# Kernel optimization log

Hardware: AMD Instinct MI355X
Metric: run time of the kernel (lower is better)

## Reference

```python
import jax, jax.numpy as jnp
import numpy as np

NUM_HEADS = 32
NUM_KV_HEADS = 8
HEAD_DIM = 128
ROPE_BASE = 10000.0


def rotate_half(x):
    half = x.shape[-1] // 2
    x1, x2 = x[..., :half], x[..., half:]
    return jnp.concatenate((-x2, x1), axis=-1)


def rope_cos_sin(position_ids, head_dim, dtype):
    # inv_freq: [head_dim/2]
    inv_freq = 1.0 / (ROPE_BASE ** (jnp.arange(0, head_dim, 2, dtype=jnp.float32) / head_dim))
    freqs = position_ids.astype(jnp.float32)[..., None] * inv_freq  # [B, S, hd/2]
    emb = jnp.concatenate((freqs, freqs), axis=-1)                  # [B, S, hd]
    # add head axis -> [B, 1, S, hd]
    return jnp.cos(emb)[:, None].astype(dtype), jnp.sin(emb)[:, None].astype(dtype)


def setup_inputs() -> dict:
    key = jax.random.key(0)
    k_x, k_q, k_k, k_v, k_o = jax.random.split(key, 5)
    B, S, H = 1, 2048, 4096
    w_scale = 0.02
    return {
        "hidden_states": jax.random.normal(k_x, (B, S, H), dtype=jnp.float32),
        "position_ids": jnp.broadcast_to(jnp.arange(S, dtype=jnp.int32), (B, S)),
        "Wq": jax.random.normal(k_q, (NUM_HEADS * HEAD_DIM, H), dtype=jnp.float32) * w_scale,
        "Wk": jax.random.normal(k_k, (NUM_KV_HEADS * HEAD_DIM, H), dtype=jnp.float32) * w_scale,
        "Wv": jax.random.normal(k_v, (NUM_KV_HEADS * HEAD_DIM, H), dtype=jnp.float32) * w_scale,
        "Wo": jax.random.normal(k_o, (H, NUM_HEADS * HEAD_DIM), dtype=jnp.float32) * w_scale,
    }


def reference(hidden_states, position_ids, Wq, Wk, Wv, Wo):
    B, S, H = hidden_states.shape
    n_rep = NUM_HEADS // NUM_KV_HEADS

    # projections (torch Linear: y = x @ W.T), reshape to [B, heads, S, hd]
    q = (hidden_states @ Wq.T).reshape(B, S, NUM_HEADS, HEAD_DIM).transpose(0, 2, 1, 3)
    k = (hidden_states @ Wk.T).reshape(B, S, NUM_KV_HEADS, HEAD_DIM).transpose(0, 2, 1, 3)
    v = (hidden_states @ Wv.T).reshape(B, S, NUM_KV_HEADS, HEAD_DIM).transpose(0, 2, 1, 3)

    cos, sin = rope_cos_sin(position_ids, HEAD_DIM, hidden_states.dtype)
    q = q * cos + rotate_half(q) * sin
    k = k * cos + rotate_half(k) * sin

    # repeat_kv: GQA expansion to [B, NUM_HEADS, S, hd]
    k = jnp.repeat(k, n_rep, axis=1)
    v = jnp.repeat(v, n_rep, axis=1)

    scale = 1.0 / jnp.sqrt(jnp.asarray(HEAD_DIM, dtype=hidden_states.dtype))
    scores = jnp.einsum('bhqd,bhkd->bhqk', q, k) * scale  # [B, H, S, S]

    # causal additive mask
    causal = jnp.tril(jnp.ones((S, S), dtype=bool))
    scores = jnp.where(causal[None, None], scores, jnp.finfo(scores.dtype).min)

    probs = jax.nn.softmax(scores, axis=-1)
    attn = jnp.einsum('bhqk,bhkd->bhqd', probs, v)         # [B, H, S, hd]
    attn = attn.transpose(0, 2, 1, 3).reshape(B, S, NUM_HEADS * HEAD_DIM)
    return attn @ Wo.T
```

## Files before the change

kernel.cpp:

```cpp
#include <hip/hip_runtime.h>
#include <hip/hip_bf16.h>
#include <stdint.h>

typedef __bf16 bf16;
typedef __attribute__((ext_vector_type(8))) __bf16 bf16x8;
typedef __attribute__((ext_vector_type(4))) __bf16 bf16x4;
typedef __attribute__((ext_vector_type(4))) float f32x4;
typedef __attribute__((ext_vector_type(16))) float f32x16;

#define S_LEN 2048
#define HDIM  4096
#define NQH   32
#define NKVH  8
#define DHEAD 128
#define QKVN  6144
#define KOFF  4096
#define VOFF  5120

__device__ __forceinline__ void gload_lds16(const bf16* g, bf16* l) {
  __builtin_amdgcn_global_load_lds(
      (const __attribute__((address_space(1))) unsigned int*)g,
      (__attribute__((address_space(3))) unsigned int*)l, 16, 0, 0);
}

__global__ __launch_bounds__(256) void cvt_f32_bf16(const float* __restrict__ in,
                                                    bf16* __restrict__ out, int n4) {
  int i = blockIdx.x * 256 + threadIdx.x;
  if (i >= n4) return;
  float4 v = ((const float4*)in)[i];
  bf16x4 ov = {(bf16)v.x, (bf16)v.y, (bf16)v.z, (bf16)v.w};
  *(bf16x4*)&out[(size_t)i * 4] = ov;
}

__global__ __launch_bounds__(256) void rope_table(const int* __restrict__ pos,
                                                  float* __restrict__ tab) {
  int idx = blockIdx.x * 256 + threadIdx.x;
  int i = idx & 63, s = idx >> 6;
  float p = (float)pos[s];
  float invf = powf(10000.0f, -(float)i * (1.0f / 64.0f));
  float ang = p * invf;
  tab[idx * 2]     = cosf(ang);
  tab[idx * 2 + 1] = sinf(ang);
}

__global__ __launch_bounds__(256) void rope_apply(bf16* __restrict__ QKV,
                                                  const float* __restrict__ tab) {
  int idx = blockIdx.x * 256 + threadIdx.x;
  int dp = idx & 63;
  int t = idx >> 6;
  int head = t % 40;
  int s = t / 40;
  float c  = tab[(s * 64 + dp) * 2];
  float sn = tab[(s * 64 + dp) * 2 + 1];
  size_t base = (size_t)s * QKVN + head * DHEAD;
  float x0 = (float)QKV[base + dp];
  float x1 = (float)QKV[base + 64 + dp];
  QKV[base + dp]      = (bf16)(x0 * c - x1 * sn);
  QKV[base + 64 + dp] = (bf16)(x1 * c + x0 * sn);
}

__global__ __launch_bounds__(256) void transpose_v(const bf16* __restrict__ QKV,
                                                   bf16* __restrict__ Vt) {
  __shared__ bf16 t[64][72];
  int tid = threadIdx.x;
  int bs = blockIdx.x * 64, bc = blockIdx.y * 64;
  int sl = tid >> 3, cb = (tid & 7) * 8;
#pragma unroll
  for (int ss = 0; ss < 64; ss += 32) {
    int s = sl + ss;
    *(bf16x8*)&t[s][cb] = *(const bf16x8*)&QKV[(size_t)(bs + s) * QKVN + VOFF + bc + cb];
  }
  __syncthreads();
  int cl = tid >> 3, sb = (tid & 7) * 8;
#pragma unroll
  for (int cc = 0; cc < 64; cc += 32) {
    int c = cl + cc;
    bf16x8 v;
#pragma unroll
    for (int k = 0; k < 8; ++k) v[k] = t[sb + k][c];
    *(bf16x8*)&Vt[(size_t)(bc + c) * S_LEN + bs + sb] = v;
  }
}

template <typename OutT>
__global__ __launch_bounds__(256) void gemm_bt(const bf16* __restrict__ A,
                                               const bf16* __restrict__ B,
                                               OutT* __restrict__ C,
                                               int M, int N, int K) {
  __shared__ bf16 At[128 * 64];
  __shared__ bf16 Bt[128 * 64];
  const int tid = threadIdx.x;
  const int w = tid >> 6, lane = tid & 63;
  const int r = lane & 15, g = lane >> 4;
  const int bm = blockIdx.y * 128, bn = blockIdx.x * 128;
  const int wm = (w >> 1) * 64, wn = (w & 1) * 64;
  f32x4 acc[4][4];
#pragma unroll
  for (int i = 0; i < 4; ++i)
#pragma unroll
    for (int j = 0; j < 4; ++j) acc[i][j] = (f32x4){0.f, 0.f, 0.f, 0.f};

  const int chunk0 = w * 256 + lane;

  for (int k0 = 0; k0 < K; k0 += 64) {
#pragma unroll
    for (int i = 0; i < 4; ++i) {
      int chunk = chunk0 + i * 64;
      int row = chunk >> 3, c8 = chunk & 7;
      int cs = ((c8 ^ (row & 7)) << 3) + k0;
      gload_lds16(&A[(size_t)(bm + row) * K + cs], &At[(w * 4 + i) * 512]);
      gload_lds16(&B[(size_t)(bn + row) * K + cs], &Bt[(w * 4 + i) * 512]);
    }
    __syncthreads();
#pragma unroll
    for (int ks = 0; ks < 2; ++ks) {
      bf16x8 af[4], bfr[4];
#pragma unroll
      for (int mi = 0; mi < 4; ++mi) {
        int row = wm + mi * 16 + r;
        af[mi] = *(const bf16x8*)&At[row * 64 + ((((ks << 2) + g) ^ (row & 7)) << 3)];
      }
#pragma unroll
      for (int nj = 0; nj < 4; ++nj) {
        int row = wn + nj * 16 + r;
        bfr[nj] = *(const bf16x8*)&Bt[row * 64 + ((((ks << 2) + g) ^ (row & 7)) << 3)];
      }
#pragma unroll
      for (int mi = 0; mi < 4; ++mi)
#pragma unroll
        for (int nj = 0; nj < 4; ++nj)
          acc[mi][nj] = __builtin_amdgcn_mfma_f32_16x16x32_bf16(af[mi], bfr[nj],
                                                                acc[mi][nj], 0, 0, 0);
    }
    __syncthreads();
  }
#pragma unroll
  for (int mi = 0; mi < 4; ++mi)
#pragma unroll
    for (int nj = 0; nj < 4; ++nj)
#pragma unroll
      for (int j = 0; j < 4; ++j) {
        int row = bm + wm + mi * 16 + g * 4 + j;
        int col = bn + wn + nj * 16 + r;
        C[(size_t)row * N + col] = (OutT)acc[mi][nj][j];
      }
}

__global__ __launch_bounds__(64, 2) void attn_kernel(const bf16* __restrict__ QKV,
                                                     const bf16* __restrict__ Vt,
                                                     bf16* __restrict__ Opart,
                                                     float* __restrict__ Mpart,
                                                     float* __restrict__ Lpart) {
  const int lane = threadIdx.x & 63;
  const int l31 = lane & 31, hi = lane >> 5;
  const int bx = blockIdx.x;
  const int kvh = bx & 7;
  const int hq = (bx >> 3) & 3;
  const int s = (bx >> 5) & 1;
  const int qblk = 63 - (bx >> 6);
  const int h = kvh * 4 + hq;
  const int q0 = qblk * 32;
  const int pid = ((h * 64 + qblk) * 2 + s);
  const float scale = 0.12751746f;

  const int nt = qblk + 1;
  const int h0 = (nt + 1) >> 1;
  const int t0 = s ? h0 : 0;
  const int t1 = s ? nt : h0;

  f32x16 o[4];
#pragma unroll
  for (int t = 0; t < 4; ++t)
#pragma unroll
    for (int r = 0; r < 16; ++r) o[t][r] = 0.f;
  float m_run = -1e30f, l_run = 0.f;

  if (t0 < t1) {
    bf16x8 qf[8];
#pragma unroll
    for (int k8 = 0; k8 < 8; ++k8) {
      bf16x8 raw = *(const bf16x8*)&QKV[(size_t)(q0 + l31) * QKVN + h * DHEAD + k8 * 16 + hi * 8];
#pragma unroll
      for (int e = 0; e < 8; ++e) qf[k8][e] = (bf16)((float)raw[e] * scale);
    }

    auto loadK = [&](bf16x8 (&kd)[8], int kv0) {
#pragma unroll
      for (int k8 = 0; k8 < 8; ++k8)
        kd[k8] = *(const bf16x8*)&QKV[(size_t)(kv0 + l31) * QKVN + KOFF +
                                      kvh * DHEAD + k8 * 16 + hi * 8];
    };

    auto process = [&](bf16x8 (&kc)[8], bf16x8 (&kn)[8], int kv0, bool pre, bool diag) {
      bf16x8 vf[8];
#pragma unroll
      for (int t = 0; t < 4; ++t) {
        const bf16* vb = &Vt[(size_t)(kvh * DHEAD + t * 32 + l31) * S_LEN + kv0 + hi * 8];
        vf[2 * t]     = *(const bf16x8*)vb;
        vf[2 * t + 1] = *(const bf16x8*)(vb + 16);
      }
      f32x16 st;
#pragma unroll
      for (int r = 0; r < 16; ++r) st[r] = 0.f;
      __builtin_amdgcn_s_setprio(1);
#pragma unroll
      for (int k8 = 0; k8 < 8; ++k8)
        st = __builtin_amdgcn_mfma_f32_32x32x16_bf16(kc[k8], qf[k8], st, 0, 0, 0);
      __builtin_amdgcn_s_setprio(0);
      if (pre) loadK(kn, kv0 + 32);
      if (diag) {
#pragma unroll
        for (int r = 0; r < 16; ++r) {
          int kvr = (r & 3) + 8 * (r >> 2) + 4 * hi;
          if (kvr > l31) st[r] = -1e30f;
        }
      }
      float pmax = st[0];
#pragma unroll
      for (int r = 1; r < 16; ++r) pmax = fmaxf(pmax, st[r]);
      pmax = fmaxf(pmax, __shfl_xor(pmax, 32));
      if (!__all(pmax - m_run <= 8.0f)) {
        float mnew = fmaxf(m_run, pmax);
        float corr = exp2f(m_run - mnew);
        m_run = mnew;
        l_run *= corr;
#pragma unroll
        for (int r = 0; r < 16; ++r) {
          float cr = __shfl(corr, (r & 3) + 8 * (r >> 2) + 4 * hi);
          o[0][r] *= cr; o[1][r] *= cr; o[2][r] *= cr; o[3][r] *= cr;
        }
      }
      float p[16], rs = 0.f;
#pragma unroll
      for (int r = 0; r < 16; ++r) { p[r] = exp2f(st[r] - m_run); rs += p[r]; }
      rs += __shfl_xor(rs, 32);
      l_run += rs;
      float sp[16];
#pragma unroll
      for (int i = 0; i < 16; ++i) sp[i] = __shfl_xor(p[i], 32);
      bf16x8 pf0, pf1;
#pragma unroll
      for (int e = 0; e < 4; ++e) {
        pf0[e]     = (bf16)(hi ? sp[4 + e]  : p[e]);
        pf0[e + 4] = (bf16)(hi ? p[4 + e]   : sp[e]);
        pf1[e]     = (bf16)(hi ? sp[12 + e] : p[8 + e]);
        pf1[e + 4] = (bf16)(hi ? p[12 + e]  : sp[8 + e]);
      }
      __builtin_amdgcn_s_setprio(1);
#pragma unroll
      for (int t = 0; t < 4; ++t) {
        o[t] = __builtin_amdgcn_mfma_f32_32x32x16_bf16(pf0, vf[2 * t],     o[t], 0, 0, 0);
        o[t] = __builtin_amdgcn_mfma_f32_32x32x16_bf16(pf1, vf[2 * t + 1], o[t], 0, 0, 0);
      }
      __builtin_amdgcn_s_setprio(0);
    };

    bf16x8 kfA[8], kfB[8];
    loadK(kfA, t0 * 32);
    int t = t0;
    while (true) {
      process(kfA, kfB, t * 32, t + 1 < t1, t == nt - 1);
      ++t; if (t >= t1) break;
      process(kfB, kfA, t * 32, t + 1 < t1, t == nt - 1);
      ++t; if (t >= t1) break;
    }
  }

  float linv = (l_run > 0.f) ? 1.0f / l_run : 0.f;
  if (hi == 0) {
    Mpart[pid * 32 + l31] = m_run;
    Lpart[pid * 32 + l31] = l_run;
  }
#pragma unroll
  for (int r = 0; r < 16; ++r) {
    int qloc = (r & 3) + 8 * (r >> 2) + 4 * hi;
    float li = __shfl(linv, qloc);
    size_t row = (size_t)pid * (32 * DHEAD) + (size_t)qloc * DHEAD;
#pragma unroll
    for (int t2 = 0; t2 < 4; ++t2)
      Opart[row + t2 * 32 + l31] = (bf16)(o[t2][r] * li);
  }
}

__global__ __launch_bounds__(256) void attn_merge(const bf16* __restrict__ Opart,
                                                  const float* __restrict__ Mpart,
                                                  const float* __restrict__ Lpart,
                                                  bf16* __restrict__ Oout) {
  const int bx = blockIdx.x;
  const int h = bx >> 6, qblk = bx & 63;
  const int tid = threadIdx.x;
  const int r = tid >> 3, cseg = (tid & 7) * 16;
  const int pid0 = bx * 2, pid1 = pid0 + 1;
  float m0 = Mpart[pid0 * 32 + r], m1 = Mpart[pid1 * 32 + r];
  float l0 = Lpart[pid0 * 32 + r], l1 = Lpart[pid1 * 32 + r];
  float M = fmaxf(m0, m1);
  float w0 = l0 * exp2f(m0 - M), w1 = l1 * exp2f(m1 - M);
  float inv = 1.0f / (w0 + w1);
  w0 *= inv; w1 *= inv;
  size_t src0 = (size_t)pid0 * (32 * DHEAD) + (size_t)r * DHEAD + cseg;
  size_t src1 = (size_t)pid1 * (32 * DHEAD) + (size_t)r * DHEAD + cseg;
  size_t dst = (size_t)(qblk * 32 + r) * HDIM + h * DHEAD + cseg;
#pragma unroll
  for (int half = 0; half < 2; ++half) {
    bf16x8 a = *(const bf16x8*)&Opart[src0 + half * 8];
    bf16x8 b = *(const bf16x8*)&Opart[src1 + half * 8];
    bf16x8 out;
#pragma unroll
    for (int e = 0; e < 8; ++e) out[e] = (bf16)(w0 * (float)a[e] + w1 * (float)b[e]);
    *(bf16x8*)&Oout[dst + half * 8] = out;
  }
}

extern "C" void kernel_launch(void* const* d_in, const int* in_sizes, int n_in,
                              void* d_out, int out_size, void* d_ws, size_t ws_size,
                              hipStream_t stream) {
  const float* X   = (const float*)d_in[0];
  const int*   pos = (const int*)d_in[1];
  const float* Wq  = (const float*)d_in[2];
  const float* Wk  = (const float*)d_in[3];
  const float* Wv  = (const float*)d_in[4];
  const float* Wo  = (const float*)d_in[5];
  float* out = (float*)d_out;
  char* ws = (char*)d_ws;

  size_t off = 0;
  bf16* Xb    = (bf16*)(ws + off); off += (size_t)2048 * 4096 * 2;
  bf16* Wqkvb = (bf16*)(ws + off); off += (size_t)6144 * 4096 * 2;
  bf16* Wob   = (bf16*)(ws + off); off += (size_t)4096 * 4096 * 2;
  bf16* QKV   = (bf16*)(ws + off); off += (size_t)2048 * 6144 * 2;
  bf16* Vt    = (bf16*)(ws + off); off += (size_t)1024 * 2048 * 2;
  bf16* attnb = (bf16*)(ws + off); off += (size_t)2048 * 4096 * 2;
  float* tab  = (float*)(ws + off); off += (size_t)2048 * 64 * 2 * 4;

  bf16*  Opart = (bf16*)Wqkvb;
  float* Mpart = (float*)((char*)Wqkvb + (size_t)4096 * 32 * 128 * 2);
  float* Lpart = Mpart + (size_t)4096 * 32;

  cvt_f32_bf16<<<2048 * 4096 / 4 / 256, 256, 0, stream>>>(X, Xb, 2048 * 4096 / 4);
  cvt_f32_bf16<<<4096 * 4096 / 4 / 256, 256, 0, stream>>>(Wq, Wqkvb, 4096 * 4096 / 4);
  cvt_f32_bf16<<<1024 * 4096 / 4 / 256, 256, 0, stream>>>(Wk, Wqkvb + (size_t)4096 * 4096,
                                                          1024 * 4096 / 4);
  cvt_f32_bf16<<<1024 * 4096 / 4 / 256, 256, 0, stream>>>(Wv, Wqkvb + (size_t)5120 * 4096,
                                                          1024 * 4096 / 4);
  cvt_f32_bf16<<<4096 * 4096 / 4 / 256, 256, 0, stream>>>(Wo, Wob, 4096 * 4096 / 4);
  rope_table<<<2048 * 64 / 256, 256, 0, stream>>>(pos, tab);
  gemm_bt<bf16><<<dim3(QKVN / 128, 2048 / 128), 256, 0, stream>>>(Xb, Wqkvb, QKV,
                                                                  2048, QKVN, 4096);
  rope_apply<<<2048 * 40 * 64 / 256, 256, 0, stream>>>(QKV, tab);
  transpose_v<<<dim3(2048 / 64, 1024 / 64), 256, 0, stream>>>(QKV, Vt);
  attn_kernel<<<4096, 64, 0, stream>>>(QKV, Vt, Opart, Mpart, Lpart);
  attn_merge<<<2048, 256, 0, stream>>>(Opart, Mpart, Lpart, attnb);
  gemm_bt<float><<<dim3(4096 / 128, 2048 / 128), 256, 0, stream>>>(attnb, Wob, out,
                                                                   2048, 4096, 4096);
}
```

Measured before the change: 416.9 us.

## Share GQA K/V tiles across four query heads via swizzled LDS double buffer

```diff
diff --git a/kernel.cpp b/kernel.cpp
--- a/kernel.cpp
+++ b/kernel.cpp
@@ -7,6 +7,7 @@
 typedef __attribute__((ext_vector_type(4))) __bf16 bf16x4;
 typedef __attribute__((ext_vector_type(4))) float f32x4;
 typedef __attribute__((ext_vector_type(16))) float f32x16;
+typedef __attribute__((ext_vector_type(4))) unsigned int uint4v;
 
 #define S_LEN 2048
 #define HDIM  4096
@@ -146,27 +147,32 @@
       }
 }
 
-__global__ __launch_bounds__(64, 2) void attn_kernel(const bf16* __restrict__ QKV,
-                                                     const bf16* __restrict__ Vt,
-                                                     bf16* __restrict__ Opart,
-                                                     float* __restrict__ Mpart,
-                                                     float* __restrict__ Lpart) {
-  const int lane = threadIdx.x & 63;
+__global__ __launch_bounds__(256) void attn_kernel(const bf16* __restrict__ QKV,
+                                                   const bf16* __restrict__ Vt,
+                                                   bf16* __restrict__ Opart,
+                                                   float* __restrict__ Mpart,
+                                                   float* __restrict__ Lpart) {
+  __shared__ bf16 Kl[2][32 * 128];
+  __shared__ bf16 Vl[2][128 * 32];
+  const int tid = threadIdx.x;
+  const int w = tid >> 6, lane = tid & 63;
   const int l31 = lane & 31, hi = lane >> 5;
   const int bx = blockIdx.x;
   const int kvh = bx & 7;
-  const int hq = (bx >> 3) & 3;
-  const int s = (bx >> 5) & 1;
-  const int qblk = 63 - (bx >> 6);
-  const int h = kvh * 4 + hq;
+  const int rem = bx >> 3;
+  const int s = rem & 1;
+  const int u = rem >> 1;
+  const int ua = u & 15, ub = u >> 4;
+  const int qblk = (ub & 1) ? ((3 - ub) * 16 + (15 - ua)) : ((3 - ub) * 16 + ua);
+  const int h = kvh * 4 + w;
   const int q0 = qblk * 32;
-  const int pid = ((h * 64 + qblk) * 2 + s);
+  const int pid = (h * 64 + qblk) * 2 + s;
   const float scale = 0.12751746f;
 
   const int nt = qblk + 1;
-  const int h0 = (nt + 1) >> 1;
-  const int t0 = s ? h0 : 0;
-  const int t1 = s ? nt : h0;
+  const int hh = (nt + 1) >> 1;
+  const int t0 = s ? hh : 0;
+  const int t1 = s ? nt : hh;
 
   f32x16 o[4];
 #pragma unroll
@@ -175,6 +181,21 @@
     for (int r = 0; r < 16; ++r) o[t][r] = 0.f;
   float m_run = -1e30f, l_run = 0.f;
 
+  auto stage = [&](int bufi, int kv0) {
+#pragma unroll
+    for (int ii = 0; ii < 2; ++ii) {
+      int ins = w * 2 + ii;
+      int kr = ins * 4 + (lane >> 4);
+      int ck = (lane & 15) ^ (kr & 15);
+      gload_lds16(&QKV[(size_t)(kv0 + kr) * QKVN + KOFF + kvh * DHEAD + ck * 8],
+                  &Kl[bufi][ins * 512]);
+      int d = ins * 16 + (lane >> 2);
+      int cv = (lane & 3) ^ (d & 3);
+      gload_lds16(&Vt[(size_t)(kvh * DHEAD + d) * S_LEN + kv0 + cv * 8],
+                  &Vl[bufi][ins * 512]);
+    }
+  };
+
   if (t0 < t1) {
     bf16x8 qf[8];
 #pragma unroll
@@ -184,31 +205,26 @@
       for (int e = 0; e < 8; ++e) qf[k8][e] = (bf16)((float)raw[e] * scale);
     }
 
-    auto loadK = [&](bf16x8 (&kd)[8], int kv0) {
-#pragma unroll
-      for (int k8 = 0; k8 < 8; ++k8)
-        kd[k8] = *(const bf16x8*)&QKV[(size_t)(kv0 + l31) * QKVN + KOFF +
-                                      kvh * DHEAD + k8 * 16 + hi * 8];
-    };
-
-    auto process = [&](bf16x8 (&kc)[8], bf16x8 (&kn)[8], int kv0, bool pre, bool diag) {
-      bf16x8 vf[8];
-#pragma unroll
-      for (int t = 0; t < 4; ++t) {
-        const bf16* vb = &Vt[(size_t)(kvh * DHEAD + t * 32 + l31) * S_LEN + kv0 + hi * 8];
-        vf[2 * t]     = *(const bf16x8*)vb;
-        vf[2 * t + 1] = *(const bf16x8*)(vb + 16);
-      }
+    stage(t0 & 1, t0 * 32);
+    __syncthreads();
+
+    for (int t = t0; t < t1; ++t) {
+      const int cur = t & 1;
+      if (t + 1 < t1) stage(cur ^ 1, (t + 1) * 32);
+
       f32x16 st;
 #pragma unroll
       for (int r = 0; r < 16; ++r) st[r] = 0.f;
       __builtin_amdgcn_s_setprio(1);
 #pragma unroll
-      for (int k8 = 0; k8 < 8; ++k8)
-        st = __builtin_amdgcn_mfma_f32_32x32x16_bf16(kc[k8], qf[k8], st, 0, 0, 0);
+      for (int k8 = 0; k8 < 8; ++k8) {
+        bf16x8 kf = *(const bf16x8*)&Kl[cur][l31 * 128 +
+                                            (((2 * k8 + hi) ^ (l31 & 15)) << 3)];
+        st = __builtin_amdgcn_mfma_f32_32x32x16_bf16(kf, qf[k8], st, 0, 0, 0);
+      }
       __builtin_amdgcn_s_setprio(0);
-      if (pre) loadK(kn, kv0 + 32);
-      if (diag) {
+
+      if (t == nt - 1) {
 #pragma unroll
         for (int r = 0; r < 16; ++r) {
           int kvr = (r & 3) + 8 * (r >> 2) + 4 * hi;
@@ -235,34 +251,32 @@
       for (int r = 0; r < 16; ++r) { p[r] = exp2f(st[r] - m_run); rs += p[r]; }
       rs += __shfl_xor(rs, 32);
       l_run += rs;
-      float sp[16];
-#pragma unroll
-      for (int i = 0; i < 16; ++i) sp[i] = __shfl_xor(p[i], 32);
-      bf16x8 pf0, pf1;
-#pragma unroll
-      for (int e = 0; e < 4; ++e) {
-        pf0[e]     = (bf16)(hi ? sp[4 + e]  : p[e]);
-        pf0[e + 4] = (bf16)(hi ? p[4 + e]   : sp[e]);
-        pf1[e]     = (bf16)(hi ? sp[12 + e] : p[8 + e]);
-        pf1[e + 4] = (bf16)(hi ? p[12 + e]  : sp[8 + e]);
-      }
+      unsigned int A[8], X[8];
+#pragma unroll
+      for (int j = 0; j < 8; ++j) {
+        unsigned short lo = __builtin_bit_cast(unsigned short, (bf16)p[2 * j]);
+        unsigned short hi16 = __builtin_bit_cast(unsigned short, (bf16)p[2 * j + 1]);
+        A[j] = (unsigned int)lo | ((unsigned int)hi16 << 16);
+      }
+#pragma unroll
+      for (int j = 0; j < 8; ++j) X[j] = __shfl_xor(A[j], 32);
+      uint4v w0v = {hi ? X[2] : A[0], hi ? X[3] : A[1],
+                    hi ? A[2] : X[0], hi ? A[3] : X[1]};
+      uint4v w1v = {hi ? X[6] : A[4], hi ? X[7] : A[5],
+                    hi ? A[6] : X[4], hi ? A[7] : X[5]};
+      bf16x8 pf0 = __builtin_bit_cast(bf16x8, w0v);
+      bf16x8 pf1 = __builtin_bit_cast(bf16x8, w1v);
       __builtin_amdgcn_s_setprio(1);
 #pragma unroll
-      for (int t = 0; t < 4; ++t) {
-        o[t] = __builtin_amdgcn_mfma_f32_32x32x16_bf16(pf0, vf[2 * t],     o[t], 0, 0, 0);
-        o[t] = __builtin_amdgcn_mfma_f32_32x32x16_bf16(pf1, vf[2 * t + 1], o[t], 0, 0, 0);
+      for (int tt = 0; tt < 4; ++tt) {
+        int dt = tt * 32 + l31;
+        bf16x8 v0 = *(const bf16x8*)&Vl[cur][dt * 32 + ((hi ^ (l31 & 3)) << 3)];
+        bf16x8 v1 = *(const bf16x8*)&Vl[cur][dt * 32 + (((2 + hi) ^ (l31 & 3)) << 3)];
+        o[tt] = __builtin_amdgcn_mfma_f32_32x32x16_bf16(pf0, v0, o[tt], 0, 0, 0);
+        o[tt] = __builtin_amdgcn_mfma_f32_32x32x16_bf16(pf1, v1, o[tt], 0, 0, 0);
       }
       __builtin_amdgcn_s_setprio(0);
-    };
-
-    bf16x8 kfA[8], kfB[8];
-    loadK(kfA, t0 * 32);
-    int t = t0;
-    while (true) {
-      process(kfA, kfB, t * 32, t + 1 < t1, t == nt - 1);
-      ++t; if (t >= t1) break;
-      process(kfB, kfA, t * 32, t + 1 < t1, t == nt - 1);
-      ++t; if (t >= t1) break;
+      __syncthreads();
     }
   }
 
@@ -348,7 +362,7 @@
                                                                   2048, QKVN, 4096);
   rope_apply<<<2048 * 40 * 64 / 256, 256, 0, stream>>>(QKV, tab);
   transpose_v<<<dim3(2048 / 64, 1024 / 64), 256, 0, stream>>>(QKV, Vt);
-  attn_kernel<<<4096, 64, 0, stream>>>(QKV, Vt, Opart, Mpart, Lpart);
+  attn_kernel<<<1024, 256, 0, stream>>>(QKV, Vt, Opart, Mpart, Lpart);
   attn_merge<<<2048, 256, 0, stream>>>(Opart, Mpart, Lpart, attnb);
   gemm_bt<float><<<dim3(4096 / 128, 2048 / 128), 256, 0, stream>>>(attnb, Wob, out,
                                                                    2048, 4096, 4096);
```

New measurement: 400.0 us. 1.04x faster.
